# Kernel tuning notes

Hardware: AMD Instinct MI355X
Metric: run time of the kernel (lower is better)

Reference implementation:

```python
import jax, jax.numpy as jnp
import numpy as np

ALPHA = 0.05  # steady-state adaptive alpha (current_step >= warmup_steps)
EPS = 1e-8    # torch cosine_similarity norm clamp

N = 8192
D = 512


def setup_inputs() -> dict:
    key = jax.random.key(0)
    k1, k2 = jax.random.split(key)
    old_emb = jax.random.normal(k1, (N, D), dtype=jnp.float32)
    new_emb = jax.random.normal(k2, (N, D), dtype=jnp.float32)
    return {"old_emb": old_emb, "new_emb": new_emb}


def _featurewise_ot(hidden_old, hidden_new, alpha):
    # nearest-neighbor match by cosine similarity (k=1 topk == argmax)
    old_n = hidden_old / jnp.maximum(jnp.linalg.norm(hidden_old, axis=1, keepdims=True), EPS)
    new_n = hidden_new / jnp.maximum(jnp.linalg.norm(hidden_new, axis=1, keepdims=True), EPS)
    sim = old_n @ new_n.T                      # [n1, n2]
    idx = jnp.argmax(sim, axis=1)              # [n1]
    expanded = hidden_new[idx]                 # [n1, d]

    # batched per-column sort-based OT alignment (replaces the python loop over d)
    h_src = jnp.sort(hidden_old, axis=0)                       # sorted old, per column
    order = jnp.argsort(expanded, axis=0)                      # idx_tgt per column
    h_tgt = jnp.take_along_axis(expanded, order, axis=0)       # sorted target, per column
    delta = alpha * (h_src - h_tgt)                            # [n1, d]
    cols = jnp.broadcast_to(jnp.arange(expanded.shape[1]), order.shape)
    update = jnp.zeros_like(expanded).at[order, cols].set(delta)  # inverse-permutation scatter
    return expanded + update


def reference(old_emb, new_emb):
    aligned_old = _featurewise_ot(old_emb, new_emb, ALPHA)
    return (1.0 - ALPHA) * new_emb + ALPHA * aligned_old
```

## Files before the change

### kernel.cpp

```cpp
#include <hip/hip_runtime.h>
#include <hip/hip_bf16.h>
#include <stdint.h>

#define NROWS 8192
#define DIM 512
#define MARGIN 0.03f
#define OVF_CAP 32

typedef unsigned long long u64;
typedef uint32_t u32;
using bf16x8 = __attribute__((ext_vector_type(8))) short;
using ushort8 = __attribute__((ext_vector_type(8))) unsigned short;
using f32x4 = __attribute__((ext_vector_type(4))) float;

__device__ __forceinline__ u32 f2o(float f){
  u32 u = __float_as_uint(f);
  return (u & 0x80000000u) ? ~u : (u | 0x80000000u);
}
__device__ __forceinline__ float o2f(u32 o){
  u32 u = (o & 0x80000000u) ? (o & 0x7FFFFFFFu) : ~o;
  return __uint_as_float(u);
}
__device__ __forceinline__ unsigned short bfbits(float f){
  __hip_bfloat16 h = __float2bfloat16(f);
  return *reinterpret_cast<unsigned short*>(&h);
}
__device__ __forceinline__ unsigned short f2o16(unsigned short b){
  return (b & 0x8000u) ? (unsigned short)~b : (unsigned short)(b | 0x8000u);
}
__device__ __forceinline__ unsigned short o2b16(unsigned short o){
  return (o & 0x8000u) ? (unsigned short)(o & 0x7FFFu) : (unsigned short)~o;
}
__device__ __forceinline__ float b16f(unsigned short b){
  u32 u = (u32)b << 16;
  return __uint_as_float(u);
}
typedef __attribute__((address_space(1))) const void gvoid;
typedef __attribute__((address_space(3))) void svoid;
__device__ __forceinline__ void gll16(const void* g, void* l){
  __builtin_amdgcn_global_load_lds((gvoid*)g, (svoid*)l, 16, 0, 0);
}

__device__ __forceinline__ int HIDX(int b){ return b + (b >> 5); }

__global__ void kconvnorm(const float* __restrict__ olde, const float* __restrict__ newe,
                          unsigned short* __restrict__ abf, unsigned short* __restrict__ bbf,
                          float* __restrict__ invn, u32* __restrict__ cnt){
  int row = blockIdx.x * 4 + (threadIdx.x >> 6);
  int lane = threadIdx.x & 63;
  if (blockIdx.x < 32) cnt[blockIdx.x * 256 + threadIdx.x] = 0u;
  bool isnew = row >= NROWS;
  int r = isnew ? row - NROWS : row;
  const float* src = (isnew ? newe : olde) + (size_t)r * DIM + lane * 8;
  unsigned short* dst = (isnew ? bbf : abf) + (size_t)r * DIM + lane * 8;
  float4 v0 = *(const float4*)src, v1 = *(const float4*)(src + 4);
  ushort8 wv = { bfbits(v0.x), bfbits(v0.y), bfbits(v0.z), bfbits(v0.w),
                 bfbits(v1.x), bfbits(v1.y), bfbits(v1.z), bfbits(v1.w) };
  *(ushort8*)dst = wv;
  if (isnew){
    float s = v0.x*v0.x + v0.y*v0.y + v0.z*v0.z + v0.w*v0.w
            + v1.x*v1.x + v1.y*v1.y + v1.z*v1.z + v1.w*v1.w;
    #pragma unroll
    for (int off = 32; off > 0; off >>= 1) s += __shfl_down(s, off);
    if (lane == 0) invn[r] = 1.0f / fmaxf(sqrtf(s), 1e-8f);
  }
}

__global__ void knorm(const float* __restrict__ x, float* __restrict__ invn,
                      u32* __restrict__ cnt){
  int row = blockIdx.x * 4 + (threadIdx.x >> 6);
  int lane = threadIdx.x & 63;
  if (threadIdx.x < 4) cnt[blockIdx.x * 4 + threadIdx.x] = 0u;
  const float4* xr = (const float4*)(x + (size_t)row * DIM);
  float s = 0.f;
  #pragma unroll
  for (int k = 0; k < 2; ++k){
    float4 v = xr[lane + 64 * k];
    s += v.x * v.x + v.y * v.y + v.z * v.z + v.w * v.w;
  }
  #pragma unroll
  for (int off = 32; off > 0; off >>= 1) s += __shfl_down(s, off);
  if (lane == 0) invn[row] = 1.0f / fmaxf(sqrtf(s), 1e-8f);
}

__device__ __forceinline__ void argmax_epilogue(
    f32x4 (&acc)[2][8], const float* __restrict__ invn,
    int m0, int n0w, int ntile, int wr, int c16, int g,
    u64* __restrict__ Tt, u64* __restrict__ ovf, u32* __restrict__ cnt){
  float invc[8];
  #pragma unroll
  for (int nj = 0; nj < 8; ++nj) invc[nj] = invn[n0w + nj * 16 + c16];
  #pragma unroll
  for (int mi = 0; mi < 2; ++mi){
    #pragma unroll
    for (int reg = 0; reg < 4; ++reg){
      float bv = -3.4e38f; int bj = 0;
      #pragma unroll
      for (int nj = 0; nj < 8; ++nj){
        float v = acc[mi][nj][reg] * invc[nj];
        if (v > bv){ bv = v; bj = nj; }
      }
      int gj = n0w + bj * 16 + c16;
      u64 pk = ((u64)f2o(bv) << 32) | (u32)(~(u32)gj);
      #pragma unroll
      for (int m = 1; m < 16; m <<= 1){
        u64 o = __shfl_xor(pk, m);
        pk = pk > o ? pk : o;
      }
      int grow = m0 + wr * 32 + mi * 16 + g * 4 + reg;
      if (c16 == 0) Tt[(size_t)grow * 64 + ntile] = pk;
      float thr = o2f((u32)(pk >> 32)) - MARGIN;
      int tj = (int)~((u32)pk);
      #pragma unroll
      for (int nj = 0; nj < 8; ++nj){
        float v = acc[mi][nj][reg] * invc[nj];
        int j = n0w + nj * 16 + c16;
        if (v >= thr && j != tj){
          u32 pos = atomicAdd(&cnt[grow], 1u);
          if (pos < OVF_CAP) ovf[(size_t)grow * OVF_CAP + pos] = ((u64)f2o(v) << 32) | (u32)j;
        }
      }
    }
  }
}

__global__ __launch_bounds__(512) void kgemm2(
    const unsigned short* __restrict__ Abf, const unsigned short* __restrict__ Bbf,
    const float* __restrict__ invn, u64* __restrict__ Tt,
    u64* __restrict__ ovf, u32* __restrict__ cnt){
  __shared__ unsigned short As[128 * 32];
  __shared__ unsigned short Bs[256 * 32];
  const int t = threadIdx.x;
  const int lane = t & 63, w = t >> 6;
  const int c16 = lane & 15, g = lane >> 4;
  const int wr = w >> 1, wc = w & 1;
  int bid = blockIdx.x;
  int xcd = bid & 7, s = bid >> 3;
  int bm = (xcd & 1) * 32 + (s >> 3);
  int bn = (xcd >> 1) * 8 + (s & 7);
  const int m0 = bm * 128, n0 = bn * 256;

  f32x4 acc[2][8];
  #pragma unroll
  for (int mi = 0; mi < 2; ++mi)
    #pragma unroll
    for (int nj = 0; nj < 8; ++nj) acc[mi][nj] = {0.f, 0.f, 0.f, 0.f};

  const int srow = t >> 2;
  const int part = t & 3;

  for (int k0 = 0; k0 < DIM; k0 += 32){
    {
      int sc = (part ^ ((srow >> 1) & 3)) * 8;
      gll16(Abf + (size_t)(m0 + srow) * DIM + k0 + sc, (void*)&As[(w * 16) * 32]);
    }
    {
      int sc = (part ^ ((srow >> 1) & 3)) * 8;
      gll16(Bbf + (size_t)(n0 + srow) * DIM + k0 + sc, (void*)&Bs[(w * 16) * 32]);
      int r2 = srow + 128;
      int sc2 = (part ^ ((r2 >> 1) & 3)) * 8;
      gll16(Bbf + (size_t)(n0 + r2) * DIM + k0 + sc2, (void*)&Bs[(128 + w * 16) * 32]);
    }
    __syncthreads();
    bf16x8 af[2], bfr[8];
    #pragma unroll
    for (int mi = 0; mi < 2; ++mi){
      int ra = wr * 32 + mi * 16 + c16;
      af[mi] = *(const bf16x8*)&As[ra * 32 + (g ^ ((ra >> 1) & 3)) * 8];
    }
    #pragma unroll
    for (int nj = 0; nj < 8; ++nj){
      int rb = wc * 128 + nj * 16 + c16;
      bfr[nj] = *(const bf16x8*)&Bs[rb * 32 + (g ^ ((rb >> 1) & 3)) * 8];
    }
    #pragma unroll
    for (int mi = 0; mi < 2; ++mi)
      #pragma unroll
      for (int nj = 0; nj < 8; ++nj)
        acc[mi][nj] = __builtin_amdgcn_mfma_f32_16x16x32_bf16(af[mi], bfr[nj], acc[mi][nj], 0, 0, 0);
    __syncthreads();
  }
  argmax_epilogue(acc, invn, m0, n0 + wc * 128, bn * 2 + wc, wr, c16, g, Tt, ovf, cnt);
}

__global__ __launch_bounds__(256) void kgemm_fb(
    const float* __restrict__ A, const float* __restrict__ B,
    const float* __restrict__ invn, u64* __restrict__ Tt,
    u64* __restrict__ ovf, u32* __restrict__ cnt){
  __shared__ short As[128 * 40];
  __shared__ short Bs[128 * 40];
  const int t = threadIdx.x;
  const int lane = t & 63, w = t >> 6;
  const int c16 = lane & 15, g = lane >> 4;
  const int m0 = blockIdx.y * 128, n0 = blockIdx.x * 128;

  f32x4 acc[2][8];
  #pragma unroll
  for (int mi = 0; mi < 2; ++mi)
    #pragma unroll
    for (int nj = 0; nj < 8; ++nj) acc[mi][nj] = {0.f, 0.f, 0.f, 0.f};

  for (int k0 = 0; k0 < DIM; k0 += 32){
    #pragma unroll
    for (int it = 0; it < 2; ++it){
      int s = t + it * 256;
      int row = s >> 2, part = s & 3;
      const float4* ga = (const float4*)(A + (size_t)(m0 + row) * DIM + k0 + part * 8);
      float4 a0 = ga[0], a1 = ga[1];
      bf16x8 ha = { (short)bfbits(a0.x), (short)bfbits(a0.y), (short)bfbits(a0.z), (short)bfbits(a0.w),
                    (short)bfbits(a1.x), (short)bfbits(a1.y), (short)bfbits(a1.z), (short)bfbits(a1.w) };
      *(bf16x8*)(&As[row * 40 + part * 8]) = ha;
      const float4* gb = (const float4*)(B + (size_t)(n0 + row) * DIM + k0 + part * 8);
      float4 b0 = gb[0], b1 = gb[1];
      bf16x8 hb = { (short)bfbits(b0.x), (short)bfbits(b0.y), (short)bfbits(b0.z), (short)bfbits(b0.w),
                    (short)bfbits(b1.x), (short)bfbits(b1.y), (short)bfbits(b1.z), (short)bfbits(b1.w) };
      *(bf16x8*)(&Bs[row * 40 + part * 8]) = hb;
    }
    __syncthreads();
    bf16x8 af[2], bfr[8];
    #pragma unroll
    for (int mi = 0; mi < 2; ++mi)
      af[mi] = *(const bf16x8*)(&As[(w * 32 + mi * 16 + c16) * 40 + g * 8]);
    #pragma unroll
    for (int nj = 0; nj < 8; ++nj)
      bfr[nj] = *(const bf16x8*)(&Bs[(nj * 16 + c16) * 40 + g * 8]);
    #pragma unroll
    for (int mi = 0; mi < 2; ++mi)
      #pragma unroll
      for (int nj = 0; nj < 8; ++nj)
        acc[mi][nj] = __builtin_amdgcn_mfma_f32_16x16x32_bf16(af[mi], bfr[nj], acc[mi][nj], 0, 0, 0);
    __syncthreads();
  }
  argmax_epilogue(acc, invn, m0, n0, blockIdx.x, w, c16, g, Tt, ovf, cnt);
}

__global__ __launch_bounds__(256) void kresolve(
    const float* __restrict__ A, const float* __restrict__ B,
    const float* __restrict__ invn, const u64* __restrict__ Tt,
    const u64* __restrict__ ovf, const u32* __restrict__ cnt,
    int* __restrict__ idx){
  const int r = blockIdx.x * 4 + (threadIdx.x >> 6);
  const int lane = threadIdx.x & 63;
  u64 e = Tt[(size_t)r * 64 + lane];
  u64 m = e;
  #pragma unroll
  for (int s = 1; s < 64; s <<= 1){ u64 o = __shfl_xor(m, s); m = m > o ? m : o; }
  float W = o2f((u32)(m >> 32)) - MARGIN;
  bool inw = o2f((u32)(e >> 32)) >= W;
  u64 bal = __ballot(inw);
  u32 nov_raw = cnt[r];
  int nov = nov_raw > OVF_CAP ? OVF_CAP : (int)nov_raw;
  u64 oe = (lane < nov) ? ovf[(size_t)r * OVF_CAP + lane] : 0ull;
  bool oin = (lane < nov) && (o2f((u32)(oe >> 32)) >= W);
  u64 bal2 = __ballot(oin);
  if (nov_raw <= OVF_CAP && __popcll(bal) == 1 && bal2 == 0ull){
    if (lane == 0) idx[r] = (int)~((u32)m);
    return;
  }
  const float* ar = A + (size_t)r * DIM;
  u64 best = 0ull;
  auto eval = [&](int j){
    const float* br = B + (size_t)j * DIM;
    float s = 0.f;
    for (int k = lane; k < DIM; k += 64) s = fmaf(ar[k], br[k], s);
    #pragma unroll
    for (int o = 32; o > 0; o >>= 1) s += __shfl_xor(s, o);
    s *= invn[j];
    u64 p = ((u64)f2o(s) << 32) | (u32)(~(u32)j);
    best = best > p ? best : p;
  };
  if (nov_raw > OVF_CAP){
    for (int j = 0; j < NROWS; ++j) eval(j);
  } else {
    u64 mm = bal;
    while (mm){
      int b = __ffsll((unsigned long long)mm) - 1;
      int j = (int)~((u32)__shfl(e, b));
      eval(j);
      mm &= mm - 1;
    }
    mm = bal2;
    while (mm){
      int b = __ffsll((unsigned long long)mm) - 1;
      int j = (int)(u32)__shfl(oe, b);
      eval(j);
      mm &= mm - 1;
    }
  }
  if (lane == 0) idx[r] = (int)~((u32)best);
}

__global__ void kexpand(const float* __restrict__ newe, const int* __restrict__ idx,
                        float* __restrict__ expd){
  int i = blockIdx.x * 2 + (threadIdx.x >> 7);
  int c = (threadIdx.x & 127) * 4;
  int j = idx[i];
  *(float4*)(expd + (size_t)i * DIM + c) =
      *(const float4*)(newe + (size_t)j * DIM + c);
}

__device__ __forceinline__ void scan8192(u32* hist, u32* wsums, int t, int lane, int w){
  u32 v[8]; u32 ts = 0;
  #pragma unroll
  for (int k = 0; k < 8; ++k){ v[k] = hist[HIDX(t * 8 + k)]; ts += v[k]; }
  u32 inc = ts;
  #pragma unroll
  for (int off = 1; off < 64; off <<= 1){
    u32 o = (u32)__shfl_up((int)inc, off);
    if (lane >= off) inc += o;
  }
  if (lane == 63) wsums[w] = inc;
  __syncthreads();
  u32 wb = 0;
  #pragma unroll
  for (int i = 0; i < 16; ++i){ u32 x = wsums[i]; if (i < w) wb += x; }
  u32 run = wb + inc - ts;
  #pragma unroll
  for (int k = 0; k < 8; ++k){ u32 x = v[k]; hist[HIDX(t * 8 + k)] = run; run += x; }
}

__global__ __launch_bounds__(1024) void ksort3(
    const float* __restrict__ olde, const float* __restrict__ newe,
    const int* __restrict__ idx, float* __restrict__ out){
  __shared__ u32 hist[8448];
  __shared__ unsigned short vals[NROWS];
  __shared__ u32 wsums[16];
  const int bid = blockIdx.x;
  const int c = (bid & 7) * 64 + (bid >> 3);
  const int t = threadIdx.x;
  const int lane = t & 63, w = t >> 6;

  #pragma unroll
  for (int k = 0; k < 8; ++k) hist[t + k * 1024] = 0;
  if (t < 256) hist[8192 + t] = 0;
  __syncthreads();
  unsigned short ob[8]; int oc[8];
  #pragma unroll
  for (int k = 0; k < 8; ++k){
    int e = t + k * 1024;
    ob[k] = bfbits(olde[(size_t)e * DIM + c]);
    oc[k] = (int)((u32)f2o16(ob[k]) >> 3);
    atomicAdd(&hist[HIDX(oc[k])], 1u);
  }
  __syncthreads();
  scan8192(hist, wsums, t, lane, w);
  __syncthreads();
  #pragma unroll
  for (int k = 0; k < 8; ++k){
    u32 pos = atomicAdd(&hist[HIDX(oc[k])], 1u);
    vals[pos] = ob[k];
  }
  __syncthreads();

  #pragma unroll
  for (int k = 0; k < 8; ++k) hist[t + k * 1024] = 0;
  if (t < 256) hist[8192 + t] = 0;
  __syncthreads();
  float ev[8]; int ec[8];
  #pragma unroll
  for (int k = 0; k < 8; ++k){
    int e = t + k * 1024;
    int j = idx[e];
    float x = newe[(size_t)j * DIM + c];
    ev[k] = x;
    ec[k] = (int)((u32)f2o16(bfbits(x)) >> 3);
    atomicAdd(&hist[HIDX(ec[k])], 1u);
  }
  __syncthreads();
  scan8192(hist, wsums, t, lane, w);
  __syncthreads();
  #pragma unroll
  for (int k = 0; k < 8; ++k){
    int e = t + k * 1024;
    u32 pos = atomicAdd(&hist[HIDX(ec[k])], 1u);
    float hsrc = b16f(vals[pos]);
    float aligned = fmaf(0.95f, ev[k], 0.05f * hsrc);
    out[(size_t)e * DIM + c] = fmaf(0.95f, newe[(size_t)e * DIM + c], 0.05f * aligned);
  }
}

template<bool HASPAY>
__device__ __forceinline__ void radix_pass_fb(
    u32* srcK, u32* srcP, u32* dstK, u32* dstP,
    u32* hist, u32* totals, u32* digitbase,
    int shift, int w, int lane, int t){
  for (int i = t; i < 4096; i += 1024) hist[i] = 0;
  __syncthreads();
  u32 kreg[8], preg[8], dloc[8];
  #pragma unroll
  for (int k = 0; k < 8; ++k){
    int e = w * 512 + k * 64 + lane;
    u32 key = srcK[e];
    if (HASPAY) preg[k] = srcP[e];
    kreg[k] = key;
    u32 d = (key >> shift) & 255u;
    u64 m = ~0ull;
    #pragma unroll
    for (int b = 0; b < 8; ++b){
      u64 bb = __ballot((d >> b) & 1u);
      m &= ((d >> b) & 1u) ? bb : ~bb;
    }
    int leader = __ffsll((unsigned long long)m) - 1;
    u32 rank = (u32)__popcll(m & ((1ull << lane) - 1ull));
    u32 cntg = (u32)__popcll(m);
    u32 old = 0;
    if (lane == leader){ old = hist[w * 256 + d]; hist[w * 256 + d] = old + cntg; }
    old = (u32)__shfl((int)old, leader);
    dloc[k] = (d << 16) | (old + rank);
  }
  __syncthreads();
  if (t < 256){
    u32 run = 0;
    #pragma unroll
    for (int ww = 0; ww < 16; ++ww){
      u32 v = hist[ww * 256 + t];
      hist[ww * 256 + t] = run;
      run += v;
    }
    totals[t] = run;
  }
  __syncthreads();
  if (t < 64){
    u32 carry = 0;
    #pragma unroll
    for (int ch = 0; ch < 4; ++ch){
      u32 v = totals[ch * 64 + t];
      u32 inc = v;
      #pragma unroll
      for (int off = 1; off < 64; off <<= 1){
        u32 o = (u32)__shfl_up((int)inc, off);
        if (t >= off) inc += o;
      }
      digitbase[ch * 64 + t] = carry + inc - v;
      carry += (u32)__shfl((int)inc, 63);
    }
  }
  __syncthreads();
  #pragma unroll
  for (int k = 0; k < 8; ++k){
    u32 d = dloc[k] >> 16, off = dloc[k] & 0xFFFFu;
    u32 dst = digitbase[d] + hist[w * 256 + d] + off;
    dstK[dst] = kreg[k];
    if (HASPAY) dstP[dst] = preg[k];
  }
  __syncthreads();
}

__global__ __launch_bounds__(1024) void ksort_fb(
    const float* __restrict__ olde, float* expd_out){
  __shared__ u32 buf0[NROWS], buf1[NROWS], pay0[NROWS], pay1[NROWS];
  __shared__ u32 hist[4096], totals[256], digitbase[256];
  const int bid = blockIdx.x;
  const int c = (bid & 7) * 64 + (bid >> 3);
  const int t = threadIdx.x;
  const int lane = t & 63, w = t >> 6;

  for (int e = t; e < NROWS; e += 1024){
    buf0[e] = f2o(expd_out[(size_t)e * DIM + c]);
    pay0[e] = (u32)e;
  }
  __syncthreads();
  radix_pass_fb<true>(buf0, pay0, buf1, pay1, hist, totals, digitbase, 0,  w, lane, t);
  radix_pass_fb<true>(buf1, pay1, buf0, pay0, hist, totals, digitbase, 8,  w, lane, t);
  radix_pass_fb<true>(buf0, pay0, buf1, pay1, hist, totals, digitbase, 16, w, lane, t);
  radix_pass_fb<true>(buf1, pay1, buf0, pay0, hist, totals, digitbase, 24, w, lane, t);
  for (int e = t; e < NROWS; e += 1024)
    buf1[e] = f2o(olde[(size_t)e * DIM + c]);
  __syncthreads();
  radix_pass_fb<false>(buf1, pay1, pay1, buf1, hist, totals, digitbase, 0,  w, lane, t);
  radix_pass_fb<false>(pay1, buf1, buf1, pay1, hist, totals, digitbase, 8,  w, lane, t);
  radix_pass_fb<false>(buf1, pay1, pay1, buf1, hist, totals, digitbase, 16, w, lane, t);
  radix_pass_fb<false>(pay1, buf1, buf1, pay1, hist, totals, digitbase, 24, w, lane, t);
  for (int e = t; e < NROWS; e += 1024){
    u32 row = pay0[e];
    float expv = o2f(buf0[e]);
    float hsrc = o2f(buf1[e]);
    float aligned = expv + 0.05f * (hsrc - expv);
    pay1[row] = __float_as_uint(0.05f * aligned);
  }
  __syncthreads();
  for (int e = t; e < NROWS; e += 1024)
    expd_out[(size_t)e * DIM + c] = __uint_as_float(pay1[e]);
}

__global__ void kfinal(const float* __restrict__ newe, float* __restrict__ out){
  size_t i = (size_t)blockIdx.x * 256 + threadIdx.x;
  float4 n4 = ((const float4*)newe)[i];
  float4 o4 = ((float4*)out)[i];
  o4.x = fmaf(0.95f, n4.x, o4.x);
  o4.y = fmaf(0.95f, n4.y, o4.y);
  o4.z = fmaf(0.95f, n4.z, o4.z);
  o4.w = fmaf(0.95f, n4.w, o4.w);
  ((float4*)out)[i] = o4;
}

extern "C" void kernel_launch(void* const* d_in, const int* in_sizes, int n_in,
                              void* d_out, int out_size, void* d_ws, size_t ws_size,
                              hipStream_t stream){
  const float* olde = (const float*)d_in[0];
  const float* newe = (const float*)d_in[1];
  float* out = (float*)d_out;
  int* idx = (int*)d_ws;
  float* invn = (float*)((char*)d_ws + 32768);

  const size_t WS_NEED = 65536 + (size_t)512 * NROWS * 2 + 65536;

  if (ws_size >= WS_NEED){
    unsigned short* Abf = (unsigned short*)d_out;
    unsigned short* Bbf = Abf + (size_t)NROWS * DIM;
    char* base = (char*)d_ws + 65536;
    u64* Tt  = (u64*)base;
    u64* ovf = (u64*)(base + (size_t)NROWS * 64 * 8);
    u32* cnt = (u32*)(base + (size_t)NROWS * 64 * 8 + (size_t)NROWS * OVF_CAP * 8);

    kconvnorm<<<2 * NROWS / 4, 256, 0, stream>>>(olde, newe, Abf, Bbf, invn, cnt);
    kgemm2<<<2048, 512, 0, stream>>>(Abf, Bbf, invn, Tt, ovf, cnt);
    kresolve<<<NROWS / 4, 256, 0, stream>>>(olde, newe, invn, Tt, ovf, cnt, idx);
    ksort3<<<DIM, 1024, 0, stream>>>(olde, newe, idx, out);
  } else {
    u64* Tt  = (u64*)d_out;
    u64* ovf = (u64*)((char*)d_out + (size_t)NROWS * 64 * 8);
    u32* cnt = (u32*)((char*)d_out + (size_t)NROWS * 64 * 8 + (size_t)NROWS * OVF_CAP * 8);

    knorm<<<NROWS / 4, 256, 0, stream>>>(newe, invn, cnt);
    kgemm_fb<<<dim3(64, 64), 256, 0, stream>>>(olde, newe, invn, Tt, ovf, cnt);
    kresolve<<<NROWS / 4, 256, 0, stream>>>(olde, newe, invn, Tt, ovf, cnt, idx);
    kexpand<<<NROWS / 2, 256, 0, stream>>>(newe, idx, out);
    ksort_fb<<<DIM, 1024, 0, stream>>>(olde, out);
    kfinal<<<NROWS * DIM / 4 / 256, 256, 0, stream>>>(newe, out);
  }
}
```

Measured before the change: 196.3 us.

## Double GEMM K-step to 64 with XOR swizzle; hoist all global loads in ksort3

Result: slower. 229.6 us (+16.9%).

```diff
diff --git a/kernel.cpp b/kernel.cpp
--- a/kernel.cpp
+++ b/kernel.cpp
@@ -27,9 +27,6 @@
 }
 __device__ __forceinline__ unsigned short f2o16(unsigned short b){
   return (b & 0x8000u) ? (unsigned short)~b : (unsigned short)(b | 0x8000u);
-}
-__device__ __forceinline__ unsigned short o2b16(unsigned short o){
-  return (o & 0x8000u) ? (unsigned short)(o & 0x7FFFu) : (unsigned short)~o;
 }
 __device__ __forceinline__ float b16f(unsigned short b){
   u32 u = (u32)b << 16;
@@ -128,8 +125,8 @@
     const unsigned short* __restrict__ Abf, const unsigned short* __restrict__ Bbf,
     const float* __restrict__ invn, u64* __restrict__ Tt,
     u64* __restrict__ ovf, u32* __restrict__ cnt){
-  __shared__ unsigned short As[128 * 32];
-  __shared__ unsigned short Bs[256 * 32];
+  __shared__ unsigned short As[128 * 64];
+  __shared__ unsigned short Bs[256 * 64];
   const int t = threadIdx.x;
   const int lane = t & 63, w = t >> 6;
   const int c16 = lane & 15, g = lane >> 4;
@@ -146,38 +143,40 @@
     #pragma unroll
     for (int nj = 0; nj < 8; ++nj) acc[mi][nj] = {0.f, 0.f, 0.f, 0.f};
 
-  const int srow = t >> 2;
-  const int part = t & 3;
-
-  for (int k0 = 0; k0 < DIM; k0 += 32){
-    {
-      int sc = (part ^ ((srow >> 1) & 3)) * 8;
-      gll16(Abf + (size_t)(m0 + srow) * DIM + k0 + sc, (void*)&As[(w * 16) * 32]);
-    }
-    {
-      int sc = (part ^ ((srow >> 1) & 3)) * 8;
-      gll16(Bbf + (size_t)(n0 + srow) * DIM + k0 + sc, (void*)&Bs[(w * 16) * 32]);
-      int r2 = srow + 128;
-      int sc2 = (part ^ ((r2 >> 1) & 3)) * 8;
-      gll16(Bbf + (size_t)(n0 + r2) * DIM + k0 + sc2, (void*)&Bs[(128 + w * 16) * 32]);
+  const int rsub = lane >> 3;
+  const int chx = (lane & 7) ^ rsub;
+
+  for (int k0 = 0; k0 < DIM; k0 += 64){
+    #pragma unroll
+    for (int q = 0; q < 2; ++q){
+      int r0 = w * 16 + q * 8;
+      gll16(Abf + (size_t)(m0 + r0 + rsub) * DIM + k0 + chx * 8, (void*)&As[r0 * 64]);
+    }
+    #pragma unroll
+    for (int q = 0; q < 4; ++q){
+      int r0 = w * 32 + q * 8;
+      gll16(Bbf + (size_t)(n0 + r0 + rsub) * DIM + k0 + chx * 8, (void*)&Bs[r0 * 64]);
     }
     __syncthreads();
-    bf16x8 af[2], bfr[8];
-    #pragma unroll
-    for (int mi = 0; mi < 2; ++mi){
-      int ra = wr * 32 + mi * 16 + c16;
-      af[mi] = *(const bf16x8*)&As[ra * 32 + (g ^ ((ra >> 1) & 3)) * 8];
-    }
-    #pragma unroll
-    for (int nj = 0; nj < 8; ++nj){
-      int rb = wc * 128 + nj * 16 + c16;
-      bfr[nj] = *(const bf16x8*)&Bs[rb * 32 + (g ^ ((rb >> 1) & 3)) * 8];
-    }
-    #pragma unroll
-    for (int mi = 0; mi < 2; ++mi)
-      #pragma unroll
-      for (int nj = 0; nj < 8; ++nj)
-        acc[mi][nj] = __builtin_amdgcn_mfma_f32_16x16x32_bf16(af[mi], bfr[nj], acc[mi][nj], 0, 0, 0);
+    #pragma unroll
+    for (int h = 0; h < 2; ++h){
+      bf16x8 af[2], bfr[8];
+      #pragma unroll
+      for (int mi = 0; mi < 2; ++mi){
+        int ra = wr * 32 + mi * 16 + c16;
+        af[mi] = *(const bf16x8*)&As[ra * 64 + (((h * 4 + g) ^ (ra & 7)) * 8)];
+      }
+      #pragma unroll
+      for (int nj = 0; nj < 8; ++nj){
+        int rb = wc * 128 + nj * 16 + c16;
+        bfr[nj] = *(const bf16x8*)&Bs[rb * 64 + (((h * 4 + g) ^ (rb & 7)) * 8)];
+      }
+      #pragma unroll
+      for (int mi = 0; mi < 2; ++mi)
+        #pragma unroll
+        for (int nj = 0; nj < 8; ++nj)
+          acc[mi][nj] = __builtin_amdgcn_mfma_f32_16x16x32_bf16(af[mi], bfr[nj], acc[mi][nj], 0, 0, 0);
+    }
     __syncthreads();
   }
   argmax_epilogue(acc, invn, m0, n0 + wc * 128, bn * 2 + wc, wr, c16, g, Tt, ovf, cnt);
@@ -330,15 +329,25 @@
   const int t = threadIdx.x;
   const int lane = t & 63, w = t >> 6;
 
+  int j_[8];
+  #pragma unroll
+  for (int k = 0; k < 8; ++k) j_[k] = idx[t + k * 1024];
+  unsigned short ob[8];
+  #pragma unroll
+  for (int k = 0; k < 8; ++k) ob[k] = bfbits(olde[(size_t)(t + k * 1024) * DIM + c]);
+  float ev[8], nv[8];
+  #pragma unroll
+  for (int k = 0; k < 8; ++k) ev[k] = newe[(size_t)j_[k] * DIM + c];
+  #pragma unroll
+  for (int k = 0; k < 8; ++k) nv[k] = newe[(size_t)(t + k * 1024) * DIM + c];
+
   #pragma unroll
   for (int k = 0; k < 8; ++k) hist[t + k * 1024] = 0;
   if (t < 256) hist[8192 + t] = 0;
   __syncthreads();
-  unsigned short ob[8]; int oc[8];
+  int oc[8];
   #pragma unroll
   for (int k = 0; k < 8; ++k){
-    int e = t + k * 1024;
-    ob[k] = bfbits(olde[(size_t)e * DIM + c]);
     oc[k] = (int)((u32)f2o16(ob[k]) >> 3);
     atomicAdd(&hist[HIDX(oc[k])], 1u);
   }
@@ -356,14 +365,10 @@
   for (int k = 0; k < 8; ++k) hist[t + k * 1024] = 0;
   if (t < 256) hist[8192 + t] = 0;
   __syncthreads();
-  float ev[8]; int ec[8];
+  int ec[8];
   #pragma unroll
   for (int k = 0; k < 8; ++k){
-    int e = t + k * 1024;
-    int j = idx[e];
-    float x = newe[(size_t)j * DIM + c];
-    ev[k] = x;
-    ec[k] = (int)((u32)f2o16(bfbits(x)) >> 3);
+    ec[k] = (int)((u32)f2o16(bfbits(ev[k])) >> 3);
     atomicAdd(&hist[HIDX(ec[k])], 1u);
   }
   __syncthreads();
@@ -375,7 +380,7 @@
     u32 pos = atomicAdd(&hist[HIDX(ec[k])], 1u);
     float hsrc = b16f(vals[pos]);
     float aligned = fmaf(0.95f, ev[k], 0.05f * hsrc);
-    out[(size_t)e * DIM + c] = fmaf(0.95f, newe[(size_t)e * DIM + c], 0.05f * aligned);
+    out[(size_t)e * DIM + c] = fmaf(0.95f, nv[k], 0.05f * aligned);
   }
 }
 
```

## Double-buffer LDS tiles in the bf16 similarity GEMM with async prefetch

Applied to the files above, without the earlier changes.

After: 191.0 us. 1.03x faster.

```diff
diff --git a/kernel.cpp b/kernel.cpp
--- a/kernel.cpp
+++ b/kernel.cpp
@@ -27,9 +27,6 @@
 }
 __device__ __forceinline__ unsigned short f2o16(unsigned short b){
   return (b & 0x8000u) ? (unsigned short)~b : (unsigned short)(b | 0x8000u);
-}
-__device__ __forceinline__ unsigned short o2b16(unsigned short o){
-  return (o & 0x8000u) ? (unsigned short)(o & 0x7FFFu) : (unsigned short)~o;
 }
 __device__ __forceinline__ float b16f(unsigned short b){
   u32 u = (u32)b << 16;
@@ -128,8 +125,8 @@
     const unsigned short* __restrict__ Abf, const unsigned short* __restrict__ Bbf,
     const float* __restrict__ invn, u64* __restrict__ Tt,
     u64* __restrict__ ovf, u32* __restrict__ cnt){
-  __shared__ unsigned short As[128 * 32];
-  __shared__ unsigned short Bs[256 * 32];
+  __shared__ unsigned short As[2][128 * 32];
+  __shared__ unsigned short Bs[2][256 * 32];
   const int t = threadIdx.x;
   const int lane = t & 63, w = t >> 6;
   const int c16 = lane & 15, g = lane >> 4;
@@ -148,38 +145,48 @@
 
   const int srow = t >> 2;
   const int part = t & 3;
-
-  for (int k0 = 0; k0 < DIM; k0 += 32){
-    {
-      int sc = (part ^ ((srow >> 1) & 3)) * 8;
-      gll16(Abf + (size_t)(m0 + srow) * DIM + k0 + sc, (void*)&As[(w * 16) * 32]);
-    }
-    {
-      int sc = (part ^ ((srow >> 1) & 3)) * 8;
-      gll16(Bbf + (size_t)(n0 + srow) * DIM + k0 + sc, (void*)&Bs[(w * 16) * 32]);
-      int r2 = srow + 128;
-      int sc2 = (part ^ ((r2 >> 1) & 3)) * 8;
-      gll16(Bbf + (size_t)(n0 + r2) * DIM + k0 + sc2, (void*)&Bs[(128 + w * 16) * 32]);
-    }
-    __syncthreads();
+  const int scq = (part ^ ((srow >> 1) & 3)) * 8;
+  const int scq2 = (part ^ (((srow + 128) >> 1) & 3)) * 8;
+
+  auto stage = [&](int b, int k0){
+    gll16(Abf + (size_t)(m0 + srow) * DIM + k0 + scq, (void*)&As[b][(w * 16) * 32]);
+    gll16(Bbf + (size_t)(n0 + srow) * DIM + k0 + scq, (void*)&Bs[b][(w * 16) * 32]);
+    gll16(Bbf + (size_t)(n0 + srow + 128) * DIM + k0 + scq2, (void*)&Bs[b][(128 + w * 16) * 32]);
+  };
+
+  auto compute = [&](int b){
     bf16x8 af[2], bfr[8];
     #pragma unroll
     for (int mi = 0; mi < 2; ++mi){
       int ra = wr * 32 + mi * 16 + c16;
-      af[mi] = *(const bf16x8*)&As[ra * 32 + (g ^ ((ra >> 1) & 3)) * 8];
+      af[mi] = *(const bf16x8*)&As[b][ra * 32 + (g ^ ((ra >> 1) & 3)) * 8];
     }
     #pragma unroll
     for (int nj = 0; nj < 8; ++nj){
       int rb = wc * 128 + nj * 16 + c16;
-      bfr[nj] = *(const bf16x8*)&Bs[rb * 32 + (g ^ ((rb >> 1) & 3)) * 8];
+      bfr[nj] = *(const bf16x8*)&Bs[b][rb * 32 + (g ^ ((rb >> 1) & 3)) * 8];
     }
     #pragma unroll
     for (int mi = 0; mi < 2; ++mi)
       #pragma unroll
       for (int nj = 0; nj < 8; ++nj)
         acc[mi][nj] = __builtin_amdgcn_mfma_f32_16x16x32_bf16(af[mi], bfr[nj], acc[mi][nj], 0, 0, 0);
-    __syncthreads();
-  }
+  };
+
+  stage(0, 0);
+  stage(1, 32);
+  #pragma unroll 1
+  for (int kt = 0; kt < 15; ++kt){
+    asm volatile("s_waitcnt vmcnt(3)" ::: "memory");
+    __builtin_amdgcn_s_barrier();
+    compute(kt & 1);
+    __builtin_amdgcn_s_barrier();
+    if (kt < 14) stage(kt & 1, (kt + 2) * 32);
+  }
+  asm volatile("s_waitcnt vmcnt(0)" ::: "memory");
+  __builtin_amdgcn_s_barrier();
+  compute(1);
+
   argmax_epilogue(acc, invn, m0, n0 + wc * 128, bn * 2 + wc, wr, c16, g, Tt, ovf, cnt);
 }
 
```
